# Optimization experiments

Hardware: AMD Instinct MI355X
Metric: run time of the kernel (lower is better)

The kernel has to match this reference:

```python
import jax, jax.numpy as jnp
import numpy as np

N = 32768          # total nodes in batch (M graphs * N_agents)
E = N * 8          # edges (k_neighbors = 8)
DIN = 16           # node_obs_dim
DE = 8             # edge_dim (rel_pos 2 + one-hot 4 + dist 1 + payoff 1)
HE = 128           # embed_hidden_size
C = 64             # TransformerConv out_channels
H = 4              # heads (concat)
HC = H * C         # 256, final node embedding dim
EPS = 1e-5


def _ln(x, g, b):
    m = x.mean(-1, keepdims=True)
    v = ((x - m) ** 2).mean(-1, keepdims=True)
    return (x - m) * jax.lax.rsqrt(v + EPS) * g + b


def _seg_softmax(s, seg, n):
    # numerically stable softmax over edges grouped by destination node
    m = jax.ops.segment_max(s, seg, num_segments=n)
    e = jnp.exp(s - m[seg])
    z = jax.ops.segment_sum(e, seg, num_segments=n)
    return e / z[seg]


def setup_inputs() -> dict:
    key = jax.random.key(0)
    ks = jax.random.split(key, 40)

    def w(i, shape):
        return jax.random.normal(ks[i], shape, jnp.float32) * 0.05

    inp = {
        "x": jax.random.normal(ks[0], (N, DIN), jnp.float32),
        "edge_index": jax.random.randint(ks[1], (2, E), 0, N, dtype=jnp.int32),
        "edge_attr": jax.random.normal(ks[2], (E, DE), jnp.float32),
        # EmbedConv: lin1 + LN + one hidden Linear + LN (embed_layer_N=1)
        "e_W1": w(3, (DIN + DE, HE)), "e_b1": jnp.zeros((HE,), jnp.float32),
        "e_g1": jnp.ones((HE,), jnp.float32), "e_be1": jnp.zeros((HE,), jnp.float32),
        "e_W2": w(4, (HE, HE)), "e_b2": jnp.zeros((HE,), jnp.float32),
        "e_g2": jnp.ones((HE,), jnp.float32), "e_be2": jnp.zeros((HE,), jnp.float32),
    }
    # Two TransformerConv layers; layer0 in=HE, layer1 in=HC (concat heads)
    for l, din in enumerate([HE, HC]):
        base = 5 + l * 6
        inp[f"l{l}_Wq"] = w(base, (din, HC));     inp[f"l{l}_bq"] = jnp.zeros((HC,), jnp.float32)
        inp[f"l{l}_Wk"] = w(base + 1, (din, HC)); inp[f"l{l}_bk"] = jnp.zeros((HC,), jnp.float32)
        inp[f"l{l}_Wv"] = w(base + 2, (din, HC)); inp[f"l{l}_bv"] = jnp.zeros((HC,), jnp.float32)
        inp[f"l{l}_We"] = w(base + 3, (DE, HC))   # lin_edge has no bias in PyG
        inp[f"l{l}_Ws"] = w(base + 4, (din, HC)); inp[f"l{l}_bs"] = jnp.zeros((HC,), jnp.float32)
    return inp


def _tconv(h, edge_attr, src, dst, Wq, bq, Wk, bk, Wv, bv, We, Ws, bs):
    q = (h @ Wq + bq).reshape(N, H, C)
    k = (h @ Wk + bk).reshape(N, H, C)
    v = (h @ Wv + bv).reshape(N, H, C)
    e = (edge_attr @ We).reshape(E, H, C)
    ke = k[src] + e                      # [E,H,C]
    ve = v[src] + e                      # [E,H,C]
    s = (q[dst] * ke).sum(-1) / np.float32(np.sqrt(C))  # [E,H]
    a = _seg_softmax(s, dst, N)          # softmax over in-edges of each dst
    out = jax.ops.segment_sum(a[..., None] * ve, dst, num_segments=N)
    return out.reshape(N, HC) + h @ Ws + bs  # root_weight skip + bias


def reference(x, edge_attr, e_W1, e_b1, e_g1, e_be1, e_W2, e_b2, e_g2, e_be2,
              l0_Wq, l0_bq, l0_Wk, l0_bk, l0_Wv, l0_bv, l0_We, l0_Ws, l0_bs,
              l1_Wq, l1_bq, l1_Wk, l1_bk, l1_Wv, l1_bv, l1_We, l1_Ws, l1_bs,
              edge_index):
    src, dst = edge_index[0], edge_index[1]
    # EmbedConv: per-edge MLP on cat(x_j, edge_attr), scatter-add to dst
    m = jnp.concatenate([x[src], edge_attr], axis=1)    # [E, DIN+DE]
    m = _ln(jax.nn.relu(m @ e_W1 + e_b1), e_g1, e_be1)
    m = _ln(jax.nn.relu(m @ e_W2 + e_b2), e_g2, e_be2)
    h = jax.ops.segment_sum(m, dst, num_segments=N)      # [N, HE]
    # Two TransformerConv layers with ReLU activations
    h = jax.nn.relu(_tconv(h, edge_attr, src, dst, l0_Wq, l0_bq, l0_Wk, l0_bk,
                           l0_Wv, l0_bv, l0_We, l0_Ws, l0_bs))
    h = jax.nn.relu(_tconv(h, edge_attr, src, dst, l1_Wq, l1_bq, l1_Wk, l1_bk,
                           l1_Wv, l1_bv, l1_We, l1_Ws, l1_bs))
    return h  # graph_aggr == 'node': [N, HC]
```

## Files before the change

### kernel.cpp

```cpp
#include <hip/hip_runtime.h>
#include <hip/hip_bf16.h>

#define NN 32768
#define NE 262144

typedef unsigned short u16;
typedef unsigned int   u32;
typedef __bf16 bf16x8 __attribute__((ext_vector_type(8)));
typedef float  f32x16 __attribute__((ext_vector_type(16)));

__device__ __forceinline__ float bf2f(u16 u){ return __uint_as_float(((u32)u)<<16); }
__device__ __forceinline__ u16 f2bf(float f){ __hip_bfloat16 h = __float2bfloat16(f); return *(u16*)&h; }
__device__ __forceinline__ float4 ldbf4(const u16* p){
  ushort4 u = *(const ushort4*)p;
  return make_float4(bf2f(u.x), bf2f(u.y), bf2f(u.z), bf2f(u.w));
}
__device__ __forceinline__ void gload16(const void* g, void* l){
  __builtin_amdgcn_global_load_lds(
      (const __attribute__((address_space(1))) void*)g,
      (__attribute__((address_space(3))) void*)l, 16, 0, 0);
}

__global__ void k_deg(const int* __restrict__ ei, int* deg){
  int e = blockIdx.x*256 + threadIdx.x;
  if (e < NE) atomicAdd(&deg[ei[NE + e]], 1);
}

__global__ void k_scan1(const int* __restrict__ deg, int* __restrict__ rowptr, int* __restrict__ bsum){
  const int t = threadIdx.x, b = blockIdx.x;
  const int i = b*256 + t;
  const int ln = t & 63, wv = t >> 6;
  int v = deg[i];
  #pragma unroll
  for (int d = 1; d < 64; d <<= 1){
    int u = __shfl_up(v, d, 64);
    if (ln >= d) v += u;
  }
  __shared__ int wsum[4];
  if (ln == 63) wsum[wv] = v;
  __syncthreads();
  int p = 0;
  #pragma unroll
  for (int w = 0; w < 4; w++) if (w < wv) p += wsum[w];
  v += p;
  rowptr[i + 1] = v;
  if (t == 255) bsum[b] = v;
}

__global__ void k_scan2(const int* __restrict__ bsum, int* __restrict__ boff){
  const int t = threadIdx.x;
  const int ln = t & 63, wv = t >> 6;
  int own = bsum[t];
  int v = own;
  #pragma unroll
  for (int d = 1; d < 64; d <<= 1){
    int u = __shfl_up(v, d, 64);
    if (ln >= d) v += u;
  }
  __shared__ int wsum[2];
  if (ln == 63) wsum[wv] = v;
  __syncthreads();
  if (wv == 1) v += wsum[0];
  boff[t] = v - own;
}

__global__ void k_scan3(int* __restrict__ rowptr, const int* __restrict__ boff){
  const int t = threadIdx.x, b = blockIdx.x;
  rowptr[1 + b*256 + t] += boff[b];
  if (b == 0 && t == 0) rowptr[0] = 0;
}

__global__ void k_fill(const int* __restrict__ ei, const int* __restrict__ rowptr,
                       int* cursor, const float* __restrict__ ea,
                       int* __restrict__ csrc, float4* __restrict__ ea_csr){
  int e = blockIdx.x*256 + threadIdx.x;
  if (e < NE){
    int d = ei[NE + e];
    int p = rowptr[d] + atomicAdd(&cursor[d], 1);
    csrc[p] = ei[e];
    float4 a = *(const float4*)&ea[(size_t)e*8];
    float4 b = *(const float4*)&ea[(size_t)e*8 + 4];
    ea_csr[(size_t)p*2]     = a;
    ea_csr[(size_t)p*2 + 1] = b;
  }
}

__global__ void k_b2p(const float* __restrict__ W2, const float* __restrict__ be1,
                      const float* __restrict__ b2, float* __restrict__ b2p){
  int f = threadIdx.x;
  float a = b2[f];
  for (int k = 0; k < 128; k++) a += be1[k]*W2[k*128 + f];
  b2p[f] = a;
}

__global__ void k_eprep(const float* __restrict__ W1, const float* __restrict__ b1,
                        const float* __restrict__ W2, const float* __restrict__ g1,
                        const float* __restrict__ b2p, __bf16* __restrict__ Ecat){
  int i = blockIdx.x*256 + threadIdx.x;
  if (i >= 2816) return;
  bf16x8 v;
  if (i < 512){
    int r = i & 31, hh = (i>>5)&1, ks = (i>>6)&1, rt = i>>7;
    int feat = rt*32 + r, k0 = ks*16 + hh*8;
    #pragma unroll
    for (int j = 0; j < 8; j++){
      int k = k0 + j;
      float val = (k < 24) ? W1[k*128 + feat] : ((k == 24) ? b1[feat] : 0.f);
      v[j] = (__bf16)val;
    }
  } else {
    int m = i - 512;
    int r = m & 31, hh = (m>>5)&1, q = m>>6;
    int ks = q % 9, rt = q / 9;
    int feat = rt*32 + r, k0 = ks*16 + hh*8;
    #pragma unroll
    for (int j = 0; j < 8; j++){
      int k = k0 + j;
      float val = (k < 128) ? g1[k]*W2[k*128 + feat] : ((k == 128) ? b2p[feat] : 0.f);
      v[j] = (__bf16)val;
    }
  }
  *(bf16x8*)&Ecat[(size_t)i*8] = v;
}

struct WPtrs { const float* w[8]; const float* b[8]; };

__global__ void k_wprep(WPtrs wp, __bf16* __restrict__ W0cat, __bf16* __restrict__ W1cat,
                        float* __restrict__ bcat0, float* __restrict__ bcat1){
  int gid = blockIdx.x*256 + threadIdx.x;
  if (gid < 16384){
    int mat = gid >> 12, v = gid & 4095;
    int colm = v & 255, q = v >> 8;
    int k0 = (q>>1)*16 + (q&1)*8;
    const float* W = wp.w[mat];
    bf16x8 vec;
    #pragma unroll
    for (int j = 0; j < 8; j++) vec[j] = (__bf16)W[(size_t)(k0+j)*256 + colm];
    *(bf16x8*)&W0cat[((size_t)q*1024 + mat*256 + colm)*8] = vec;
  } else if (gid < 49152){
    int g = gid - 16384;
    int mat = g >> 13, v = g & 8191;
    int colm = v & 255, q = v >> 8;
    int k0 = (q>>1)*16 + (q&1)*8;
    const float* W = wp.w[4+mat];
    bf16x8 vec;
    #pragma unroll
    for (int j = 0; j < 8; j++) vec[j] = (__bf16)W[(size_t)(k0+j)*256 + colm];
    *(bf16x8*)&W1cat[((size_t)q*1024 + mat*256 + colm)*8] = vec;
  } else if (gid < 51200){
    int g = gid - 49152;
    if (g < 1024) bcat0[g] = wp.b[g>>8][g&255];
    else { int h = g-1024; bcat1[h] = wp.b[4 + (h>>8)][h&255]; }
  }
}

__global__ __launch_bounds__(256, 1) void k_embed(
    const float* __restrict__ x, const float4* __restrict__ ea_csr,
    const int* __restrict__ csrc, const int* __restrict__ rowptr,
    const __bf16* __restrict__ Ecat,
    const float* __restrict__ g2, const float* __restrict__ be2,
    u16* __restrict__ h0b)
{
  __shared__ alignas(16) __bf16 sE[2816*8];
  __shared__ float sg2[128], sbe2[128];
  const int t = threadIdx.x;
  const int wv = t >> 6, ln = t & 63, hi = ln >> 5, c32 = ln & 31;

  #pragma unroll
  for (int k = 0; k < 11; k++){
    int base = k*256 + wv*64;
    gload16(Ecat + (size_t)(base + ln)*8, &sE[(size_t)base*8]);
  }
  if (t < 128){ sg2[t] = g2[t]; sbe2[t] = be2[t]; }
  asm volatile("s_waitcnt vmcnt(0)" ::: "memory");
  __syncthreads();

  const int d   = (blockIdx.x*4 + wv)*32 + c32;
  const int rp  = rowptr[d];
  const int deg = rowptr[d+1] - rp;
  int md = deg;
  #pragma unroll
  for (int m = 1; m < 32; m <<= 1) md = max(md, __shfl_xor(md, m, 32));

  f32x16 hacc[4] = {};

  bool vc = deg > 0;
  int p0 = vc ? rp : 0;
  int sc = csrc[p0];
  float4 xa = *(const float4*)&x[(size_t)sc*16 + hi*8];
  float4 xb = *(const float4*)&x[(size_t)sc*16 + hi*8 + 4];
  float4 ga = ea_csr[(size_t)p0*2];
  float4 gb = ea_csr[(size_t)p0*2 + 1];

  for (int j = 0; j < md; j++){
    const float vm = vc ? 1.f : 0.f;
    bf16x8 b1f0, b1f1;
    {
      float xv[8]; *(float4*)&xv[0] = xa; *(float4*)&xv[4] = xb;
      #pragma unroll
      for (int q = 0; q < 8; q++) b1f0[q] = (__bf16)(xv[q]*vm);
      float evv[8]; *(float4*)&evv[0] = ga; *(float4*)&evv[4] = gb;
      #pragma unroll
      for (int q = 0; q < 8; q++)
        b1f1[q] = (__bf16)(hi ? ((q == 0) ? vm : 0.f) : evv[q]*vm);
    }

    bool vn = (j + 1) < deg;
    int pn = vn ? (rp + j + 1) : 0;
    int sn = csrc[pn];
    float4 xan = *(const float4*)&x[(size_t)sn*16 + hi*8];
    float4 xbn = *(const float4*)&x[(size_t)sn*16 + hi*8 + 4];
    float4 gan = ea_csr[(size_t)pn*2];
    float4 gbn = ea_csr[(size_t)pn*2 + 1];

    f32x16 a1[4] = {};
    #pragma unroll
    for (int ks = 0; ks < 2; ks++)
      #pragma unroll
      for (int rt = 0; rt < 4; rt++){
        bf16x8 af = *(const bf16x8*)&sE[((((rt*2 + ks)*2 + hi)*32) + c32)*8];
        a1[rt] = __builtin_amdgcn_mfma_f32_32x32x16_bf16(af, ks ? b1f1 : b1f0, a1[rt], 0, 0, 0);
      }

    {
      float s1 = 0.f, s2 = 0.f;
      #pragma unroll
      for (int rt = 0; rt < 4; rt++)
        #pragma unroll
        for (int rg = 0; rg < 16; rg++){
          float v = fmaxf(a1[rt][rg], 0.f);
          a1[rt][rg] = v; s1 += v; s2 += v*v;
        }
      s1 += __shfl_xor(s1, 32, 64);
      s2 += __shfl_xor(s2, 32, 64);
      float mean = s1*(1.f/128.f);
      float rs = rsqrtf(s2*(1.f/128.f) - mean*mean + 1e-5f);
      #pragma unroll
      for (int rt = 0; rt < 4; rt++)
        #pragma unroll
        for (int rg = 0; rg < 16; rg++)
          a1[rt][rg] = (a1[rt][rg] - mean)*rs;
    }

    f32x16 a2[4] = {};
    #pragma unroll
    for (int ks = 0; ks < 8; ks++){
      const int tt = ks >> 1, bb = (ks & 1)*8;
      float snd[4], rcv[4];
      #pragma unroll
      for (int q = 0; q < 4; q++)
        snd[q] = hi ? a1[tt][bb + q] : a1[tt][bb + 4 + q];
      #pragma unroll
      for (int q = 0; q < 4; q++)
        rcv[q] = __shfl_xor(snd[q], 32, 64);
      bf16x8 bf;
      #pragma unroll
      for (int q = 0; q < 4; q++){
        float lo = hi ? rcv[q] : a1[tt][bb + q];
        float hh = hi ? a1[tt][bb + 4 + q] : rcv[q];
        bf[q]     = (__bf16)lo;
        bf[4 + q] = (__bf16)hh;
      }
      #pragma unroll
      for (int rt = 0; rt < 4; rt++){
        bf16x8 af = *(const bf16x8*)&sE[(512 + (((rt*9 + ks)*2 + hi)*32) + c32)*8];
        a2[rt] = __builtin_amdgcn_mfma_f32_32x32x16_bf16(af, bf, a2[rt], 0, 0, 0);
      }
    }
    {
      bf16x8 bf;
      #pragma unroll
      for (int q = 0; q < 8; q++)
        bf[q] = (__bf16)((!hi && q == 0) ? vm : 0.f);
      #pragma unroll
      for (int rt = 0; rt < 4; rt++){
        bf16x8 af = *(const bf16x8*)&sE[(512 + (((rt*9 + 8)*2 + hi)*32) + c32)*8];
        a2[rt] = __builtin_amdgcn_mfma_f32_32x32x16_bf16(af, bf, a2[rt], 0, 0, 0);
      }
    }

    {
      float s1 = 0.f, s2 = 0.f;
      #pragma unroll
      for (int rt = 0; rt < 4; rt++)
        #pragma unroll
        for (int rg = 0; rg < 16; rg++){
          float v = fmaxf(a2[rt][rg], 0.f);
          a2[rt][rg] = v; s1 += v; s2 += v*v;
        }
      s1 += __shfl_xor(s1, 32, 64);
      s2 += __shfl_xor(s2, 32, 64);
      float mean = s1*(1.f/128.f);
      float rs = rsqrtf(s2*(1.f/128.f) - mean*mean + 1e-5f);
      #pragma unroll
      for (int rt = 0; rt < 4; rt++)
        #pragma unroll
        for (int rg = 0; rg < 16; rg++)
          hacc[rt][rg] += (a2[rt][rg] - mean)*rs;
    }

    vc = vn;
    xa = xan; xb = xbn; ga = gan; gb = gbn;
  }

  const float dd = (float)deg;
  #pragma unroll
  for (int rt = 0; rt < 4; rt++)
    #pragma unroll
    for (int q = 0; q < 4; q++){
      int fb = rt*32 + 8*q + 4*hi;
      ushort4 o;
      o.x = f2bf(sg2[fb+0]*hacc[rt][q*4+0] + dd*sbe2[fb+0]);
      o.y = f2bf(sg2[fb+1]*hacc[rt][q*4+1] + dd*sbe2[fb+1]);
      o.z = f2bf(sg2[fb+2]*hacc[rt][q*4+2] + dd*sbe2[fb+2]);
      o.w = f2bf(sg2[fb+3]*hacc[rt][q*4+3] + dd*sbe2[fb+3]);
      *(ushort4*)&h0b[(size_t)d*128 + fb] = o;
    }
}

template<int K>
__global__ __launch_bounds__(256) void k_qkvs2(const u16* __restrict__ A,
    const __bf16* __restrict__ Wcat, const float* __restrict__ bcat,
    u16* __restrict__ qo, u16* __restrict__ kvb, u16* __restrict__ so)
{
  __shared__ alignas(16) __bf16 sA[2][1024*8];
  __shared__ alignas(16) __bf16 sB[2][1024*8];
  const int t = threadIdx.x;
  const int swz = (blockIdx.x & 7)*256 + (blockIdx.x >> 3);
  const int r0 = (swz >> 3)*128, c0 = (swz & 7)*128;
  const int wv = t >> 6, ln = t & 63, hi = ln >> 5, c32 = ln & 31;
  const int wr = wv >> 1, wc = wv & 1;
  const int NCH = K/64;

  auto stage = [&](int kc, int b){
    #pragma unroll
    for (int ii = 0; ii < 4; ii++){
      int v = ii*256 + wv*64 + ln;
      int r = v & 31, hh = (v>>5)&1, ks = (v>>6)&3, rt = v>>8;
      gload16(A + (size_t)(r0 + rt*32 + r)*K + kc*64 + ks*16 + hh*8,
              &sA[b][(size_t)(ii*256 + wv*64)*8]);
    }
    #pragma unroll
    for (int ii = 0; ii < 4; ii++){
      int v = ii*256 + wv*64 + ln;
      int col = v & 127, q = v >> 7;
      gload16(Wcat + ((size_t)(kc*8 + q)*1024 + c0 + col)*8,
              &sB[b][(size_t)(ii*256 + wv*64)*8]);
    }
  };

  stage(0, 0);
  f32x16 acc[2][2] = {};
  for (int kc = 0; kc < NCH; kc++){
    asm volatile("s_waitcnt vmcnt(0)" ::: "memory");
    __syncthreads();
    if (kc + 1 < NCH) stage(kc + 1, (kc + 1) & 1);
    const __bf16* cA = sA[kc & 1];
    const __bf16* cB = sB[kc & 1];
    #pragma unroll
    for (int ks = 0; ks < 4; ks++){
      bf16x8 af0 = *(const bf16x8*)&cA[((((wr*2+0)*4 + ks)*2 + hi)*32 + c32)*8];
      bf16x8 af1 = *(const bf16x8*)&cA[((((wr*2+1)*4 + ks)*2 + hi)*32 + c32)*8];
      bf16x8 bf0 = *(const bf16x8*)&cB[(((ks*2 + hi)*128) + wc*64 + c32)*8];
      bf16x8 bf1 = *(const bf16x8*)&cB[(((ks*2 + hi)*128) + wc*64 + 32 + c32)*8];
      acc[0][0] = __builtin_amdgcn_mfma_f32_32x32x16_bf16(af0, bf0, acc[0][0], 0, 0, 0);
      acc[0][1] = __builtin_amdgcn_mfma_f32_32x32x16_bf16(af0, bf1, acc[0][1], 0, 0, 0);
      acc[1][0] = __builtin_amdgcn_mfma_f32_32x32x16_bf16(af1, bf0, acc[1][0], 0, 0, 0);
      acc[1][1] = __builtin_amdgcn_mfma_f32_32x32x16_bf16(af1, bf1, acc[1][1], 0, 0, 0);
    }
  }

  u16* omp; int rstride; int vadd = -1;
  if (c0 < 256)      { omp = qo;  rstride = 256; }
  else if (c0 < 512) { omp = kvb; rstride = 512; vadd = 0; }
  else if (c0 < 768) { omp = kvb; rstride = 512; vadd = 4; }
  else               { omp = so;  rstride = 256; }
  const int cb = c0 & 255;
  #pragma unroll
  for (int ci = 0; ci < 2; ci++){
    int colm = cb + wc*64 + ci*32 + c32;
    int coff = (vadd >= 0) ? (((colm >> 2) << 3) + vadd + (colm & 3)) : colm;
    float bb = bcat[c0 + wc*64 + ci*32 + c32];
    #pragma unroll
    for (int ri = 0; ri < 2; ri++){
      #pragma unroll
      for (int rg = 0; rg < 16; rg++){
        int row = r0 + (wr*2 + ri)*32 + (rg&3) + 8*(rg>>2) + 4*hi;
        omp[(size_t)row*rstride + coff] = f2bf(acc[ri][ci][rg] + bb);
      }
    }
  }
}

template<bool OBF>
__global__ __launch_bounds__(256) void k_attn(
    const int* __restrict__ csrc, const int* __restrict__ rowptr,
    const float4* __restrict__ ea_csr, const float* __restrict__ We,
    const u16* __restrict__ qb, const u16* __restrict__ kvb,
    const u16* __restrict__ skb, void* __restrict__ outp)
{
  __shared__ float sWe[8*256];
  const int t = threadIdx.x;
  for (int i = t; i < 2048; i += 256) sWe[i] = We[i];
  __syncthreads();

  const float* eaf = (const float*)ea_csr;
  const int wv = t >> 6, ln = t & 63;
  const int f = (ln >> 4)*64 + (ln & 15)*4;
  const int kvo = ((ln >> 4)*16 + (ln & 15))*8;
  const int iown = ln & 7;
  const int gbase = ln & ~15;
  const int gw = blockIdx.x*4 + wv, nW = gridDim.x*4;

#define ATT_PRE(RX, EX, jj) do{                                            \
      int sj_ = ((jj) < 64) ? __shfl(sidx, (jj), 64) : csrc[rp + (jj)];    \
      RX = *(const int4*)&kvb[(size_t)sj_*512 + kvo];                      \
      EX = eaf[(size_t)(rp + (jj))*8 + iown];                              \
    }while(0)

#define ATT_STEP(RX, EX) do{                                               \
      float kx0 = bf2f((u16)(RX.x & 0xffff)), kx1 = bf2f((u16)(((u32)RX.x)>>16)); \
      float kx2 = bf2f((u16)(RX.y & 0xffff)), kx3 = bf2f((u16)(((u32)RX.y)>>16)); \
      float vx0 = bf2f((u16)(RX.z & 0xffff)), vx1 = bf2f((u16)(((u32)RX.z)>>16)); \
      float vx2 = bf2f((u16)(RX.w & 0xffff)), vx3 = bf2f((u16)(((u32)RX.w)>>16)); \
      float spp = qv.x*kx0 + qv.y*kx1 + qv.z*kx2 + qv.w*kx3 + EX*wqsel;    \
      spp += __shfl_xor(spp, 1, 64); spp += __shfl_xor(spp, 2, 64);        \
      spp += __shfl_xor(spp, 4, 64); spp += __shfl_xor(spp, 8, 64);        \
      float nm = fmaxf(m, spp);                                            \
      float sc_ = __expf(m - nm);                                          \
      float pp = __expf(spp - nm);                                         \
      l = l*sc_ + pp;                                                      \
      o0 = o0*sc_ + pp*vx0; o1 = o1*sc_ + pp*vx1;                          \
      o2 = o2*sc_ + pp*vx2; o3 = o3*sc_ + pp*vx3;                          \
      weal = weal*sc_ + pp*EX;                                             \
      m = nm;                                                              \
    }while(0)

  for (int d = gw; d < NN; d += nW){
    const int rp = rowptr[d];
    const int dg = rowptr[d+1] - rp;
    float4 qv = ldbf4(qb + (size_t)d*256 + f);
    qv.x *= 0.125f; qv.y *= 0.125f; qv.z *= 0.125f; qv.w *= 0.125f;
    float4 sv = ldbf4(skb + (size_t)d*256 + f);

    float wqsel = 0.f;
    #pragma unroll
    for (int i = 0; i < 8; i++){
      float4 w = *(const float4*)&sWe[i*256 + f];
      float p = qv.x*w.x + qv.y*w.y + qv.z*w.z + qv.w*w.w;
      p += __shfl_xor(p, 1, 64); p += __shfl_xor(p, 2, 64);
      p += __shfl_xor(p, 4, 64); p += __shfl_xor(p, 8, 64);
      if ((ln & 15) == i) wqsel = p;
    }

    float m = -INFINITY, l = 0.f, o0 = 0, o1 = 0, o2 = 0, o3 = 0, weal = 0.f;

    if (dg > 0){
      int sidx = (ln < dg) ? csrc[rp + ln] : 0;
      int4 rA, rB, rC, rD; float eA, eB, eC, eD;
      ATT_PRE(rA, eA, 0);
      if (dg > 1) ATT_PRE(rB, eB, 1);
      if (dg > 2) ATT_PRE(rC, eC, 2);
      if (dg > 3) ATT_PRE(rD, eD, 3);

      int j = 0;
      while (j < dg){
        ATT_STEP(rA, eA); if (j + 4 < dg) ATT_PRE(rA, eA, j + 4); if (++j >= dg) break;
        ATT_STEP(rB, eB); if (j + 4 < dg) ATT_PRE(rB, eB, j + 4); if (++j >= dg) break;
        ATT_STEP(rC, eC); if (j + 4 < dg) ATT_PRE(rC, eC, j + 4); if (++j >= dg) break;
        ATT_STEP(rD, eD); if (j + 4 < dg) ATT_PRE(rD, eD, j + 4); ++j;
      }
    }

    float il = (l > 0.f) ? 1.f/l : 0.f;
    float ec0 = 0, ec1 = 0, ec2 = 0, ec3 = 0;
    #pragma unroll
    for (int i = 0; i < 8; i++){
      float wi = __shfl(weal, gbase + i, 64);
      float4 w = *(const float4*)&sWe[i*256 + f];
      ec0 += wi*w.x; ec1 += wi*w.y; ec2 += wi*w.z; ec3 += wi*w.w;
    }
    o0 = fmaxf((o0 + ec0)*il + sv.x, 0.f);
    o1 = fmaxf((o1 + ec1)*il + sv.y, 0.f);
    o2 = fmaxf((o2 + ec2)*il + sv.z, 0.f);
    o3 = fmaxf((o3 + ec3)*il + sv.w, 0.f);
    if constexpr (OBF){
      ushort4 o; o.x = f2bf(o0); o.y = f2bf(o1); o.z = f2bf(o2); o.w = f2bf(o3);
      *(ushort4*)((u16*)outp + (size_t)d*256 + f) = o;
    } else {
      *(float4*)((float*)outp + (size_t)d*256 + f) = make_float4(o0, o1, o2, o3);
    }
  }
#undef ATT_PRE
#undef ATT_STEP
}

extern "C" void kernel_launch(void* const* d_in, const int* in_sizes, int n_in,
                              void* d_out, int out_size, void* d_ws, size_t ws_size,
                              hipStream_t stream)
{
  (void)in_sizes; (void)n_in; (void)out_size; (void)ws_size;
  const float* x   = (const float*)d_in[0];
  const int*   ei  = (const int*)  d_in[1];
  const float* ea  = (const float*)d_in[2];
  const float* eW1 = (const float*)d_in[3];
  const float* eb1 = (const float*)d_in[4];
  const float* eg1 = (const float*)d_in[5];
  const float* ebe1= (const float*)d_in[6];
  const float* eW2 = (const float*)d_in[7];
  const float* eb2 = (const float*)d_in[8];
  const float* eg2 = (const float*)d_in[9];
  const float* ebe2= (const float*)d_in[10];

  char* ws = (char*)d_ws;
  const size_t MB = (size_t)1 << 20;
  const size_t KB = (size_t)1 << 10;
  int*   deg    = (int*)(ws);
  int*   cursor = (int*)(ws + 128*KB);
  int*   rowptr = (int*)(ws + 256*KB);
  int*   bsum   = (int*)(ws + 400*KB);
  int*   boff   = (int*)(ws + 402*KB);
  float* b2p    = (float*)(ws + 404*KB);
  int*   csrc   = (int*)(ws + 1*MB);
  float4* ea_csr= (float4*)(ws + 4*MB);
  u16*   qb     = (u16*)(ws + 20*MB);
  u16*   kvb    = (u16*)(ws + 36*MB);
  u16*   skb    = (u16*)(ws + 68*MB);
  u16*   h1     = (u16*)(ws + 84*MB);
  u16*   h0b    = (u16*)(ws + 100*MB);
  __bf16* W0cat = (__bf16*)(ws + 108*MB);
  __bf16* W1cat = (__bf16*)(ws + 109*MB);
  float* bcat0  = (float*)(ws + 110*MB);
  float* bcat1  = (float*)(ws + 110*MB + 64*KB);
  __bf16* Ecat  = (__bf16*)(ws + 111*MB);

  hipMemsetAsync(deg, 0, 256*KB, stream);

  k_deg  <<<NE/256, 256, 0, stream>>>(ei, deg);
  k_scan1<<<128,    256, 0, stream>>>(deg, rowptr, bsum);
  k_scan2<<<1,      128, 0, stream>>>(bsum, boff);
  k_scan3<<<128,    256, 0, stream>>>(rowptr, boff);
  k_fill <<<NE/256, 256, 0, stream>>>(ei, rowptr, cursor, ea, csrc, ea_csr);
  k_b2p  <<<1,      128, 0, stream>>>(eW2, ebe1, eb2, b2p);
  k_eprep<<<11,     256, 0, stream>>>(eW1, eb1, eW2, eg1, b2p, Ecat);

  WPtrs wp;
  wp.w[0] = (const float*)d_in[11]; wp.b[0] = (const float*)d_in[12];
  wp.w[1] = (const float*)d_in[13]; wp.b[1] = (const float*)d_in[14];
  wp.w[2] = (const float*)d_in[15]; wp.b[2] = (const float*)d_in[16];
  wp.w[3] = (const float*)d_in[18]; wp.b[3] = (const float*)d_in[19];
  wp.w[4] = (const float*)d_in[20]; wp.b[4] = (const float*)d_in[21];
  wp.w[5] = (const float*)d_in[22]; wp.b[5] = (const float*)d_in[23];
  wp.w[6] = (const float*)d_in[24]; wp.b[6] = (const float*)d_in[25];
  wp.w[7] = (const float*)d_in[27]; wp.b[7] = (const float*)d_in[28];
  k_wprep<<<200, 256, 0, stream>>>(wp, W0cat, W1cat, bcat0, bcat1);

  k_embed<<<NN/128, 256, 0, stream>>>(x, ea_csr, csrc, rowptr, Ecat, eg2, ebe2, h0b);

  k_qkvs2<128><<<2048, 256, 0, stream>>>(h0b, W0cat, bcat0, qb, kvb, skb);
  k_attn<true><<<NN/4, 256, 0, stream>>>(csrc, rowptr, ea_csr, (const float*)d_in[17],
                                         qb, kvb, skb, (void*)h1);
  k_qkvs2<256><<<2048, 256, 0, stream>>>(h1, W1cat, bcat1, qb, kvb, skb);
  k_attn<false><<<NN/4, 256, 0, stream>>>(csrc, rowptr, ea_csr, (const float*)d_in[26],
                                          qb, kvb, skb, d_out);
}
```

Measured before the change: 335.5 us.

## Fold Wq·We into GEMM, degree-sort embed nodes, drop GEMM double buffering

Precomputes a fused Wq·We matrix (scaled by 1/8) as a ninth 128-column tile in the QKVS GEMM. The per-node q·We projections then come out of the matmul, replacing the eight shuffle reductions in the attention kernel. Adds a degree histogram, scan and scatter that build a permutation so the embed kernel groups nodes of similar degree per wave, reducing divergence from looping to the max degree. Also removes double-buffered LDS staging in the GEMM in favour of a single buffer, which may lose load/compute overlap. The q·We terms are now rounded to bf16.

```diff
diff --git a/kernel.cpp b/kernel.cpp
--- a/kernel.cpp
+++ b/kernel.cpp
@@ -85,6 +85,44 @@
   }
 }
 
+__global__ void k_hist(const int* __restrict__ deg, int* ghist){
+  __shared__ int lh[64];
+  const int t = threadIdx.x;
+  if (t < 64) lh[t] = 0;
+  __syncthreads();
+  int dg = min(deg[blockIdx.x*256 + t], 63);
+  atomicAdd(&lh[dg], 1);
+  __syncthreads();
+  if (t < 64 && lh[t]) atomicAdd(&ghist[t], lh[t]);
+}
+
+__global__ void k_hoff(const int* __restrict__ ghist, int* __restrict__ goff){
+  const int t = threadIdx.x;
+  int v = ghist[t];
+  int s = v;
+  #pragma unroll
+  for (int d = 1; d < 64; d <<= 1){
+    int u = __shfl_up(s, d, 64);
+    if (t >= d) s += u;
+  }
+  goff[t] = s - v;
+}
+
+__global__ void k_scatter(const int* __restrict__ deg, const int* __restrict__ goff,
+                          int* gcur, int* __restrict__ perm){
+  __shared__ int lh[64], lbase[64];
+  const int t = threadIdx.x;
+  if (t < 64) lh[t] = 0;
+  __syncthreads();
+  const int n = blockIdx.x*256 + t;
+  const int dg = min(deg[n], 63);
+  int lrank = atomicAdd(&lh[dg], 1);
+  __syncthreads();
+  if (t < 64) lbase[t] = lh[t] ? atomicAdd(&gcur[t], lh[t]) : 0;
+  __syncthreads();
+  perm[goff[dg] + lbase[dg] + lrank] = n;
+}
+
 __global__ void k_b2p(const float* __restrict__ W2, const float* __restrict__ be1,
                       const float* __restrict__ b2, float* __restrict__ b2p){
   int f = threadIdx.x;
@@ -136,7 +174,7 @@
     bf16x8 vec;
     #pragma unroll
     for (int j = 0; j < 8; j++) vec[j] = (__bf16)W[(size_t)(k0+j)*256 + colm];
-    *(bf16x8*)&W0cat[((size_t)q*1024 + mat*256 + colm)*8] = vec;
+    *(bf16x8*)&W0cat[((size_t)q*1152 + mat*256 + colm)*8] = vec;
   } else if (gid < 49152){
     int g = gid - 16384;
     int mat = g >> 13, v = g & 8191;
@@ -146,7 +184,7 @@
     bf16x8 vec;
     #pragma unroll
     for (int j = 0; j < 8; j++) vec[j] = (__bf16)W[(size_t)(k0+j)*256 + colm];
-    *(bf16x8*)&W1cat[((size_t)q*1024 + mat*256 + colm)*8] = vec;
+    *(bf16x8*)&W1cat[((size_t)q*1152 + mat*256 + colm)*8] = vec;
   } else if (gid < 51200){
     int g = gid - 49152;
     if (g < 1024) bcat0[g] = wp.b[g>>8][g&255];
@@ -154,10 +192,42 @@
   }
 }
 
+__global__ void k_mprep(const float* __restrict__ Wq, const float* __restrict__ bq,
+                        const float* __restrict__ We, __bf16* __restrict__ Wcat,
+                        float* __restrict__ bcat, int KK){
+  int gid = blockIdx.x*256 + threadIdx.x;
+  int nv = (KK/8)*128;
+  if (gid < nv){
+    int col = gid & 127, qv_ = gid >> 7;
+    int k0 = (qv_>>1)*16 + (qv_&1)*8;
+    bf16x8 v;
+    if (col < 32){
+      int h = col >> 3, i = col & 7;
+      #pragma unroll
+      for (int j = 0; j < 8; j++){
+        float a = 0.f;
+        for (int c = 0; c < 64; c++)
+          a += Wq[(size_t)(k0+j)*256 + h*64 + c]*We[i*256 + h*64 + c];
+        v[j] = (__bf16)(0.125f*a);
+      }
+    } else {
+      #pragma unroll
+      for (int j = 0; j < 8; j++) v[j] = (__bf16)0.f;
+    }
+    *(bf16x8*)&Wcat[((size_t)qv_*1152 + 1024 + col)*8] = v;
+  }
+  if (gid < 32){
+    int h = gid >> 3, i = gid & 7;
+    float a = 0.f;
+    for (int c = 0; c < 64; c++) a += bq[h*64 + c]*We[i*256 + h*64 + c];
+    bcat[1024 + gid] = 0.125f*a;
+  }
+}
+
 __global__ __launch_bounds__(256, 1) void k_embed(
     const float* __restrict__ x, const float4* __restrict__ ea_csr,
     const int* __restrict__ csrc, const int* __restrict__ rowptr,
-    const __bf16* __restrict__ Ecat,
+    const int* __restrict__ perm, const __bf16* __restrict__ Ecat,
     const float* __restrict__ g2, const float* __restrict__ be2,
     u16* __restrict__ h0b)
 {
@@ -175,7 +245,7 @@
   asm volatile("s_waitcnt vmcnt(0)" ::: "memory");
   __syncthreads();
 
-  const int d   = (blockIdx.x*4 + wv)*32 + c32;
+  const int d   = perm[(blockIdx.x*4 + wv)*32 + c32];
   const int rp  = rowptr[d];
   const int deg = rowptr[d+1] - rp;
   int md = deg;
@@ -321,48 +391,42 @@
 template<int K>
 __global__ __launch_bounds__(256) void k_qkvs2(const u16* __restrict__ A,
     const __bf16* __restrict__ Wcat, const float* __restrict__ bcat,
-    u16* __restrict__ qo, u16* __restrict__ kvb, u16* __restrict__ so)
+    u16* __restrict__ qo, u16* __restrict__ kvb, u16* __restrict__ so,
+    u16* __restrict__ wqe)
 {
-  __shared__ alignas(16) __bf16 sA[2][1024*8];
-  __shared__ alignas(16) __bf16 sB[2][1024*8];
+  __shared__ alignas(16) __bf16 sA[1024*8];
+  __shared__ alignas(16) __bf16 sB[1024*8];
   const int t = threadIdx.x;
-  const int swz = (blockIdx.x & 7)*256 + (blockIdx.x >> 3);
-  const int r0 = (swz >> 3)*128, c0 = (swz & 7)*128;
+  const int swz = (blockIdx.x & 7)*288 + (blockIdx.x >> 3);
+  const int r0 = (swz / 9)*128, c0 = (swz % 9)*128;
   const int wv = t >> 6, ln = t & 63, hi = ln >> 5, c32 = ln & 31;
   const int wr = wv >> 1, wc = wv & 1;
-  const int NCH = K/64;
-
-  auto stage = [&](int kc, int b){
+
+  f32x16 acc[2][2] = {};
+  for (int kc = 0; kc < K/64; kc++){
+    __syncthreads();
     #pragma unroll
     for (int ii = 0; ii < 4; ii++){
       int v = ii*256 + wv*64 + ln;
       int r = v & 31, hh = (v>>5)&1, ks = (v>>6)&3, rt = v>>8;
       gload16(A + (size_t)(r0 + rt*32 + r)*K + kc*64 + ks*16 + hh*8,
-              &sA[b][(size_t)(ii*256 + wv*64)*8]);
+              &sA[(size_t)(ii*256 + wv*64)*8]);
     }
     #pragma unroll
     for (int ii = 0; ii < 4; ii++){
       int v = ii*256 + wv*64 + ln;
       int col = v & 127, q = v >> 7;
-      gload16(Wcat + ((size_t)(kc*8 + q)*1024 + c0 + col)*8,
-              &sB[b][(size_t)(ii*256 + wv*64)*8]);
-    }
-  };
-
-  stage(0, 0);
-  f32x16 acc[2][2] = {};
-  for (int kc = 0; kc < NCH; kc++){
+      gload16(Wcat + ((size_t)(kc*8 + q)*1152 + c0 + col)*8,
+              &sB[(size_t)(ii*256 + wv*64)*8]);
+    }
     asm volatile("s_waitcnt vmcnt(0)" ::: "memory");
     __syncthreads();
-    if (kc + 1 < NCH) stage(kc + 1, (kc + 1) & 1);
-    const __bf16* cA = sA[kc & 1];
-    const __bf16* cB = sB[kc & 1];
     #pragma unroll
     for (int ks = 0; ks < 4; ks++){
-      bf16x8 af0 = *(const bf16x8*)&cA[((((wr*2+0)*4 + ks)*2 + hi)*32 + c32)*8];
-      bf16x8 af1 = *(const bf16x8*)&cA[((((wr*2+1)*4 + ks)*2 + hi)*32 + c32)*8];
-      bf16x8 bf0 = *(const bf16x8*)&cB[(((ks*2 + hi)*128) + wc*64 + c32)*8];
-      bf16x8 bf1 = *(const bf16x8*)&cB[(((ks*2 + hi)*128) + wc*64 + 32 + c32)*8];
+      bf16x8 af0 = *(const bf16x8*)&sA[((((wr*2+0)*4 + ks)*2 + hi)*32 + c32)*8];
+      bf16x8 af1 = *(const bf16x8*)&sA[((((wr*2+1)*4 + ks)*2 + hi)*32 + c32)*8];
+      bf16x8 bf0 = *(const bf16x8*)&sB[(((ks*2 + hi)*128) + wc*64 + c32)*8];
+      bf16x8 bf1 = *(const bf16x8*)&sB[(((ks*2 + hi)*128) + wc*64 + 32 + c32)*8];
       acc[0][0] = __builtin_amdgcn_mfma_f32_32x32x16_bf16(af0, bf0, acc[0][0], 0, 0, 0);
       acc[0][1] = __builtin_amdgcn_mfma_f32_32x32x16_bf16(af0, bf1, acc[0][1], 0, 0, 0);
       acc[1][0] = __builtin_amdgcn_mfma_f32_32x32x16_bf16(af1, bf0, acc[1][0], 0, 0, 0);
@@ -370,17 +434,20 @@
     }
   }
 
-  u16* omp; int rstride; int vadd = -1;
-  if (c0 < 256)      { omp = qo;  rstride = 256; }
-  else if (c0 < 512) { omp = kvb; rstride = 512; vadd = 0; }
-  else if (c0 < 768) { omp = kvb; rstride = 512; vadd = 4; }
-  else               { omp = so;  rstride = 256; }
+  const int tile = c0 >> 7;
+  u16* omp; int rstride; int vadd = -1; bool wq8 = false;
+  if (tile < 2)      { omp = qo;  rstride = 256; }
+  else if (tile < 4) { omp = kvb; rstride = 512; vadd = 0; }
+  else if (tile < 6) { omp = kvb; rstride = 512; vadd = 4; }
+  else if (tile < 8) { omp = so;  rstride = 256; }
+  else               { omp = wqe; rstride = 32; wq8 = true; }
   const int cb = c0 & 255;
   #pragma unroll
   for (int ci = 0; ci < 2; ci++){
-    int colm = cb + wc*64 + ci*32 + c32;
+    int colm = (wq8 ? 0 : cb) + wc*64 + ci*32 + c32;
     int coff = (vadd >= 0) ? (((colm >> 2) << 3) + vadd + (colm & 3)) : colm;
     float bb = bcat[c0 + wc*64 + ci*32 + c32];
+    if (wq8 && colm >= 32) continue;
     #pragma unroll
     for (int ri = 0; ri < 2; ri++){
       #pragma unroll
@@ -397,7 +464,8 @@
     const int* __restrict__ csrc, const int* __restrict__ rowptr,
     const float4* __restrict__ ea_csr, const float* __restrict__ We,
     const u16* __restrict__ qb, const u16* __restrict__ kvb,
-    const u16* __restrict__ skb, void* __restrict__ outp)
+    const u16* __restrict__ skb, const u16* __restrict__ wqe,
+    void* __restrict__ outp)
 {
   __shared__ float sWe[8*256];
   const int t = threadIdx.x;
@@ -443,15 +511,8 @@
     qv.x *= 0.125f; qv.y *= 0.125f; qv.z *= 0.125f; qv.w *= 0.125f;
     float4 sv = ldbf4(skb + (size_t)d*256 + f);
 
-    float wqsel = 0.f;
-    #pragma unroll
-    for (int i = 0; i < 8; i++){
-      float4 w = *(const float4*)&sWe[i*256 + f];
-      float p = qv.x*w.x + qv.y*w.y + qv.z*w.z + qv.w*w.w;
-      p += __shfl_xor(p, 1, 64); p += __shfl_xor(p, 2, 64);
-      p += __shfl_xor(p, 4, 64); p += __shfl_xor(p, 8, 64);
-      if ((ln & 15) == i) wqsel = p;
-    }
+    float wqsel = ((ln & 15) < 8)
+                ? bf2f(wqe[(size_t)d*32 + (ln >> 4)*8 + (ln & 7)]) : 0.f;
 
     float m = -INFINITY, l = 0.f, o0 = 0, o1 = 0, o2 = 0, o3 = 0, weal = 0.f;
 
@@ -521,6 +582,10 @@
   int*   bsum   = (int*)(ws + 400*KB);
   int*   boff   = (int*)(ws + 402*KB);
   float* b2p    = (float*)(ws + 404*KB);
+  int*   ghist  = (int*)(ws + 408*KB);
+  int*   gcur   = (int*)(ws + 412*KB);
+  int*   goff   = (int*)(ws + 416*KB);
+  int*   perm   = (int*)(ws + 512*KB);
   int*   csrc   = (int*)(ws + 1*MB);
   float4* ea_csr= (float4*)(ws + 4*MB);
   u16*   qb     = (u16*)(ws + 20*MB);
@@ -533,14 +598,19 @@
   float* bcat0  = (float*)(ws + 110*MB);
   float* bcat1  = (float*)(ws + 110*MB + 64*KB);
   __bf16* Ecat  = (__bf16*)(ws + 111*MB);
+  u16*   wqeb   = (u16*)(ws + 112*MB);
 
   hipMemsetAsync(deg, 0, 256*KB, stream);
+  hipMemsetAsync(ghist, 0, 12*KB, stream);
 
   k_deg  <<<NE/256, 256, 0, stream>>>(ei, deg);
   k_scan1<<<128,    256, 0, stream>>>(deg, rowptr, bsum);
   k_scan2<<<1,      128, 0, stream>>>(bsum, boff);
   k_scan3<<<128,    256, 0, stream>>>(rowptr, boff);
   k_fill <<<NE/256, 256, 0, stream>>>(ei, rowptr, cursor, ea, csrc, ea_csr);
+  k_hist <<<NN/256, 256, 0, stream>>>(deg, ghist);
+  k_hoff <<<1,       64, 0, stream>>>(ghist, goff);
+  k_scatter<<<NN/256,256, 0, stream>>>(deg, goff, gcur, perm);
   k_b2p  <<<1,      128, 0, stream>>>(eW2, ebe1, eb2, b2p);
   k_eprep<<<11,     256, 0, stream>>>(eW1, eb1, eW2, eg1, b2p, Ecat);
 
@@ -554,13 +624,17 @@
   wp.w[6] = (const float*)d_in[24]; wp.b[6] = (const float*)d_in[25];
   wp.w[7] = (const float*)d_in[27]; wp.b[7] = (const float*)d_in[28];
   k_wprep<<<200, 256, 0, stream>>>(wp, W0cat, W1cat, bcat0, bcat1);
-
-  k_embed<<<NN/128, 256, 0, stream>>>(x, ea_csr, csrc, rowptr, Ecat, eg2, ebe2, h0b);
-
-  k_qkvs2<128><<<2048, 256, 0, stream>>>(h0b, W0cat, bcat0, qb, kvb, skb);
+  k_mprep<<<8,  256, 0, stream>>>((const float*)d_in[11], (const float*)d_in[12],
+                                  (const float*)d_in[17], W0cat, bcat0, 128);
+  k_mprep<<<16, 256, 0, stream>>>((const float*)d_in[20], (const float*)d_in[21],
+                                  (const float*)d_in[26], W1cat, bcat1, 256);
+
+  k_embed<<<NN/128, 256, 0, stream>>>(x, ea_csr, csrc, rowptr, perm, Ecat, eg2, ebe2, h0b);
+
+  k_qkvs2<128><<<2304, 256, 0, stream>>>(h0b, W0cat, bcat0, qb, kvb, skb, wqeb);
   k_attn<true><<<NN/4, 256, 0, stream>>>(csrc, rowptr, ea_csr, (const float*)d_in[17],
-                                         qb, kvb, skb, (void*)h1);
-  k_qkvs2<256><<<2048, 256, 0, stream>>>(h1, W1cat, bcat1, qb, kvb, skb);
+                                         qb, kvb, skb, wqeb, (void*)h1);
+  k_qkvs2<256><<<2304, 256, 0, stream>>>(h1, W1cat, bcat1, qb, kvb, skb, wqeb);
   k_attn<false><<<NN/4, 256, 0, stream>>>(csrc, rowptr, ea_csr, (const float*)d_in[26],
-                                          qb, kvb, skb, d_out);
-}
+                                          qb, kvb, skb, wqeb, d_out);
+}
```

New measurement: 365.4 us. 8.9% more time.
